# Performance work log

Hardware: AMD Instinct MI355X
Metric: run time of the kernel (lower is better)

## Reference

```python
import jax, jax.numpy as jnp
import numpy as np

B, S, D = 2, 2048, 1024
H = 16
DH = D // H


def setup_inputs() -> dict:
    key = jax.random.key(0)
    ks = jax.random.split(key, 6)
    scale = 1.0 / np.sqrt(D)
    x = jax.random.normal(ks[0], (B, S, D), dtype=jnp.float32)
    Wq = jax.random.normal(ks[1], (D, D), dtype=jnp.float32) * scale
    Wk = jax.random.normal(ks[2], (D, D), dtype=jnp.float32) * scale
    Wv = jax.random.normal(ks[3], (D, D), dtype=jnp.float32) * scale
    Wo = jax.random.normal(ks[4], (D, D), dtype=jnp.float32) * scale
    bo = jax.random.normal(ks[5], (D,), dtype=jnp.float32) * 0.01
    return {"x": x, "Wq": Wq, "Wk": Wk, "Wv": Wv, "Wo": Wo, "bo": bo}


def reference(x, Wq, Wk, Wv, Wo, bo):
    b, t, _ = x.shape
    # project and split heads: [b, h, t, dh]
    q = (x @ Wq).reshape(b, t, H, DH).transpose(0, 2, 1, 3)
    k = (x @ Wk).reshape(b, t, H, DH).transpose(0, 2, 1, 3)
    v = (x @ Wv).reshape(b, t, H, DH).transpose(0, 2, 1, 3)
    scores = jnp.einsum('bhqd,bhkd->bhqk', q, k)
    causal = jnp.triu(jnp.ones((t, t), dtype=bool), k=1)
    scores = jnp.where(causal, -jnp.inf, scores)
    attn = jax.nn.softmax(scores / np.sqrt(DH), axis=-1)
    ctx = jnp.einsum('bhqk,bhkd->bhqd', attn, v)
    ctx = ctx.transpose(0, 2, 1, 3).reshape(b, t, D)
    return ctx @ Wo + bo
```

## Files before the change

kernel.cpp:

```cpp
#include <hip/hip_runtime.h>
#include <hip/hip_bf16.h>

#define B 2
#define S 2048
#define D 1024
#define NH 16
#define DH 64
#define M (B*S)
#define BQ 64
#define BK 64
#define KSCALE 0.18033688011112042f

typedef __hip_bfloat16 bf16;
typedef __attribute__((ext_vector_type(8))) short frag_ab;
typedef __attribute__((ext_vector_type(4))) float frag_cd;
typedef unsigned long long ull;

__device__ __forceinline__ void gload_lds16(const bf16* g, bf16* l) {
    __builtin_amdgcn_global_load_lds((const __attribute__((address_space(1))) unsigned int*)g,
                                     (__attribute__((address_space(3))) unsigned int*)l,
                                     16, 0, 0);
}

__global__ __launch_bounds__(256) void prep(const float* __restrict__ x,  bf16* __restrict__ xb,
                                            const float* __restrict__ W0, const float* __restrict__ W1,
                                            const float* __restrict__ W2, const float* __restrict__ W3,
                                            bf16* __restrict__ T0, bf16* __restrict__ T1,
                                            bf16* __restrict__ T2, bf16* __restrict__ T3) {
    if (blockIdx.z == 4) {
        const int l = blockIdx.y * 32 + blockIdx.x;
        int i = (l * 256 + threadIdx.x) * 4;
#pragma unroll
        for (int rep = 0; rep < 4; rep++, i += 1024 * 256 * 4) {
            const float4 v = *(const float4*)(x + i);
            __align__(8) bf16 t4[4] = {__float2bfloat16(v.x), __float2bfloat16(v.y),
                                       __float2bfloat16(v.z), __float2bfloat16(v.w)};
            *(ull*)(xb + i) = *(const ull*)t4;
        }
        return;
    }
    const float* src; bf16* dst;
    switch (blockIdx.z) {
        case 0: src = W0; dst = T0; break;
        case 1: src = W1; dst = T1; break;
        case 2: src = W2; dst = T2; break;
        default: src = W3; dst = T3; break;
    }
    __shared__ float t[32][33];
    const int tx = threadIdx.x & 31, ty = threadIdx.x >> 5;
    const int c0 = blockIdx.x * 32, r0 = blockIdx.y * 32;
#pragma unroll
    for (int i = 0; i < 4; i++)
        t[ty + 8 * i][tx] = src[(size_t)(r0 + ty + 8 * i) * D + c0 + tx];
    __syncthreads();
#pragma unroll
    for (int i = 0; i < 4; i++)
        dst[(size_t)(c0 + ty + 8 * i) * D + r0 + tx] = __float2bfloat16(t[tx][ty + 8 * i]);
}

__global__ __launch_bounds__(256) void gemm_qkv_all(const bf16* __restrict__ A, const bf16* __restrict__ Bt,
                                                    bf16* __restrict__ Qb, bf16* __restrict__ Kb,
                                                    bf16* __restrict__ Vt_g) {
    __shared__ __align__(16) bf16 As[128 * BK];
    __shared__ __align__(16) bf16 Bs[128 * BK];
    const int tid = threadIdx.x, wave = tid >> 6, lane = tid & 63;
    const int r16 = lane & 15, quad = lane >> 4;
    const int row0 = blockIdx.y * 128;
    const int col0 = blockIdx.x * 128;
    const int wm = (wave & 1) * 64, wn = (wave >> 1) * 64;

    frag_cd acc[4][4];
#pragma unroll
    for (int mt = 0; mt < 4; mt++)
#pragma unroll
        for (int nt = 0; nt < 4; nt++) acc[mt][nt] = frag_cd{0.f, 0.f, 0.f, 0.f};

    for (int k0 = 0; k0 < D; k0 += BK) {
        __syncthreads();
#pragma unroll
        for (int j = 0; j < 4; j++) {
            const int s = wave * 256 + j * 64 + lane;
            const int r = s >> 3;
            const int c = (s ^ r) & 7;
            gload_lds16(A  + (size_t)(row0 + r) * D + k0 + c * 8, &As[(wave * 256 + j * 64) * 8]);
            gload_lds16(Bt + (size_t)(col0 + r) * D + k0 + c * 8, &Bs[(wave * 256 + j * 64) * 8]);
        }
        __syncthreads();

        frag_ab af[4][2], bf[4][2];
#pragma unroll
        for (int mt = 0; mt < 4; mt++) {
            const int row = wm + mt * 16 + r16;
#pragma unroll
            for (int ks = 0; ks < 2; ks++)
                af[mt][ks] = *(const frag_ab*)&As[row * 64 + (((ks * 4 + quad) ^ (row & 7)) * 8)];
        }
#pragma unroll
        for (int nt = 0; nt < 4; nt++) {
            const int row = wn + nt * 16 + r16;
#pragma unroll
            for (int ks = 0; ks < 2; ks++)
                bf[nt][ks] = *(const frag_ab*)&Bs[row * 64 + (((ks * 4 + quad) ^ (row & 7)) * 8)];
        }
#pragma unroll
        for (int mt = 0; mt < 4; mt++)
#pragma unroll
            for (int nt = 0; nt < 4; nt++)
#pragma unroll
                for (int ks = 0; ks < 2; ks++)
                    acc[mt][nt] = __builtin_amdgcn_mfma_f32_16x16x32_bf16(
                        af[mt][ks], bf[nt][ks], acc[mt][nt], 0, 0, 0);
    }

    const int third = col0 >> 10;
    if (third < 2) {
        bf16* Out = (third == 0) ? Qb : Kb;
        const float sc = (third == 0) ? KSCALE : 1.f;
#pragma unroll
        for (int mt = 0; mt < 4; mt++)
#pragma unroll
            for (int nt = 0; nt < 4; nt++) {
                const int cl = (col0 + wn + nt * 16 + r16) & 1023;
#pragma unroll
                for (int rg = 0; rg < 4; rg++) {
                    const int row = row0 + wm + mt * 16 + quad * 4 + rg;
                    Out[(size_t)row * D + cl] = __float2bfloat16(acc[mt][nt][rg] * sc);
                }
            }
    } else {
        const int bb = row0 >> 11;
        const int sb0 = (row0 & 2047) + wm;
#pragma unroll
        for (int mt = 0; mt < 4; mt++)
#pragma unroll
            for (int nt = 0; nt < 4; nt++) {
                const int c  = (col0 + wn + nt * 16 + r16) - 2048;
                const int hh = c >> 6, dl = c & 63;
                const int sb = sb0 + mt * 16 + quad * 4;
                __align__(8) bf16 t4[4];
#pragma unroll
                for (int rg = 0; rg < 4; rg++) t4[rg] = __float2bfloat16(acc[mt][nt][rg]);
                *(ull*)(Vt_g + (((size_t)bb * 16 + hh) * 64 + dl) * S + sb) = *(const ull*)t4;
            }
    }
}

__global__ __launch_bounds__(256) void attn_mfma(const bf16* __restrict__ Q,
                                                 const bf16* __restrict__ K,
                                                 const bf16* __restrict__ Vg,
                                                 bf16* __restrict__ Ctx) {
    __shared__ __align__(16) bf16 Ks[2][BK * DH];
    __shared__ __align__(16) bf16 Vt[2][BK * DH];
    __shared__ __align__(16) bf16 Qs[BQ * DH];
    bf16* Ps = Qs;

    const int tid = threadIdx.x, wave = tid >> 6, lane = tid & 63;
    const int r16 = lane & 15, quad = lane >> 4;
    const int bh = blockIdx.x, jy = blockIdx.y;
    const int qt = (jy < 16) ? jy : 47 - jy;
    const int b = bh >> 4, h = bh & 15;
    const size_t base  = (size_t)b * S * D + (size_t)h * DH;
    const size_t vbase = (size_t)bh * DH * S;
    const int q0 = qt * BQ;
    const int qwave = q0 + wave * 16;
    const int nkt = qt + 1;

#pragma unroll
    for (int j = 0; j < 2; j++) {
        const int s = wave * 128 + j * 64 + lane;
        const int r = s >> 3, c = (s ^ r) & 7;
        gload_lds16(Q + base + (size_t)(q0 + r) * D + c * 8, &Qs[(wave * 128 + j * 64) * 8]);
    }
#pragma unroll
    for (int j = 0; j < 2; j++) {
        const int s = wave * 128 + j * 64 + lane;
        const int r = s >> 3, c = (s ^ r) & 7;
        gload_lds16(K  + base  + (size_t)r * D + c * 8, &Ks[0][(wave * 128 + j * 64) * 8]);
        gload_lds16(Vg + vbase + (size_t)r * S + c * 8, &Vt[0][(wave * 128 + j * 64) * 8]);
    }
    __syncthreads();

    frag_ab qf[2];
    {
        const int row = wave * 16 + r16;
#pragma unroll
        for (int ks = 0; ks < 2; ks++)
            qf[ks] = *(const frag_ab*)&Qs[row * 64 + (((ks * 4 + quad) ^ (row & 7)) * 8)];
    }

    const frag_ab onesf = {(short)0x3F80, (short)0x3F80, (short)0x3F80, (short)0x3F80,
                           (short)0x3F80, (short)0x3F80, (short)0x3F80, (short)0x3F80};

    frag_cd Oacc[4];
#pragma unroll
    for (int nd = 0; nd < 4; nd++) Oacc[nd] = frag_cd{0.f, 0.f, 0.f, 0.f};
    frag_cd Lacc = frag_cd{0.f, 0.f, 0.f, 0.f};

    for (int kt = 0; kt < nkt; kt++) {
        const int k0  = kt * BK;
        const int cur = kt & 1;

        if (kt + 1 < nkt) {
            const int kn = k0 + BK;
#pragma unroll
            for (int j = 0; j < 2; j++) {
                const int s = wave * 128 + j * 64 + lane;
                const int r = s >> 3, c = (s ^ r) & 7;
                gload_lds16(K  + base  + (size_t)(kn + r) * D + c * 8,
                            &Ks[cur ^ 1][(wave * 128 + j * 64) * 8]);
                gload_lds16(Vg + vbase + (size_t)r * S + kn + c * 8,
                            &Vt[cur ^ 1][(wave * 128 + j * 64) * 8]);
            }
        }

        {
            frag_ab ka[4][2];
#pragma unroll
            for (int mk = 0; mk < 4; mk++) {
                const int row = mk * 16 + r16;
#pragma unroll
                for (int ks = 0; ks < 2; ks++)
                    ka[mk][ks] = *(const frag_ab*)&Ks[cur][row * 64 + (((ks * 4 + quad) ^ (row & 7)) * 8)];
            }
            const bool domask = (k0 + BK - 1 > qwave);

            frag_cd Sc[4];
#pragma unroll
            for (int mk = 0; mk < 4; mk++) {
                Sc[mk] = frag_cd{0.f, 0.f, 0.f, 0.f};
#pragma unroll
                for (int ks = 0; ks < 2; ks++)
                    Sc[mk] = __builtin_amdgcn_mfma_f32_16x16x32_bf16(
                        ka[mk][ks], qf[ks], Sc[mk], 0, 0, 0);
            }
            const int qg = qwave + r16;
            const int qrow = wave * 16 + r16;
#pragma unroll
            for (int mk = 0; mk < 4; mk++) {
                __align__(8) bf16 t4[4];
#pragma unroll
                for (int rg = 0; rg < 4; rg++) {
                    float sv = Sc[mk][rg];
                    if (domask) {
                        const int keyg = k0 + mk * 16 + quad * 4 + rg;
                        sv = (keyg <= qg) ? sv : -1e30f;
                    }
                    t4[rg] = __float2bfloat16(__builtin_amdgcn_exp2f(sv));
                }
                const int g2 = (mk * 4 + quad) ^ r16;
                *(ull*)&Ps[qrow * 64 + g2 * 4] = *(const ull*)t4;
            }


            frag_ab pa[2], vb[4][2];
#pragma unroll
            for (int ks = 0; ks < 2; ks++) {
                const int gb = ks * 8 + quad * 2;
                union { ull u[2]; frag_ab f; } t;
                t.u[0] = *(const ull*)&Ps[qrow * 64 + ((gb    ) ^ r16) * 4];
                t.u[1] = *(const ull*)&Ps[qrow * 64 + ((gb + 1) ^ r16) * 4];
                pa[ks] = t.f;
            }
#pragma unroll
            for (int nd = 0; nd < 4; nd++) {
                const int row = nd * 16 + r16;
#pragma unroll
                for (int ks = 0; ks < 2; ks++)
                    vb[nd][ks] = *(const frag_ab*)&Vt[cur][row * 64 + (((ks * 4 + quad) ^ (row & 7)) * 8)];
            }
#pragma unroll
            for (int nd = 0; nd < 4; nd++)
#pragma unroll
                for (int ks = 0; ks < 2; ks++)
                    Oacc[nd] = __builtin_amdgcn_mfma_f32_16x16x32_bf16(
                        vb[nd][ks], pa[ks], Oacc[nd], 0, 0, 0);
#pragma unroll
            for (int ks = 0; ks < 2; ks++)
                Lacc = __builtin_amdgcn_mfma_f32_16x16x32_bf16(
                    onesf, pa[ks], Lacc, 0, 0, 0);
        }

        __syncthreads();
    }

    {
        const float invl = 1.f / Lacc[0];
        const int qg = qwave + r16;
#pragma unroll
        for (int nd = 0; nd < 4; nd++) {
            __align__(8) bf16 t4[4];
#pragma unroll
            for (int rg = 0; rg < 4; rg++)
                t4[rg] = __float2bfloat16(Oacc[nd][rg] * invl);
            *(ull*)(Ctx + base + (size_t)qg * D + nd * 16 + quad * 4) = *(const ull*)t4;
        }
    }
}

__global__ __launch_bounds__(256) void gemm_out64(const bf16* __restrict__ A, const bf16* __restrict__ Bt,
                                                  const float* __restrict__ bias, float* __restrict__ Out) {
    __shared__ __align__(16) bf16 As[2][64 * BK];
    __shared__ __align__(16) bf16 Bs[2][128 * BK];
    const int tid = threadIdx.x, wave = tid >> 6, lane = tid & 63;
    const int r16 = lane & 15, quad = lane >> 4;
    const int row0 = blockIdx.y * 64;
    const int col0 = blockIdx.x * 128;
    const int wm = (wave & 1) * 32, wn = (wave >> 1) * 64;

    frag_cd acc[2][4];
#pragma unroll
    for (int mt = 0; mt < 2; mt++)
#pragma unroll
        for (int nt = 0; nt < 4; nt++) acc[mt][nt] = frag_cd{0.f, 0.f, 0.f, 0.f};

#pragma unroll
    for (int j = 0; j < 2; j++) {
        const int s = wave * 128 + j * 64 + lane;
        const int r = s >> 3, c = (s ^ r) & 7;
        gload_lds16(A + (size_t)(row0 + r) * D + c * 8, &As[0][(wave * 128 + j * 64) * 8]);
    }
#pragma unroll
    for (int j = 0; j < 4; j++) {
        const int s = wave * 256 + j * 64 + lane;
        const int r = s >> 3, c = (s ^ r) & 7;
        gload_lds16(Bt + (size_t)(col0 + r) * D + c * 8, &Bs[0][(wave * 256 + j * 64) * 8]);
    }
    __syncthreads();

    for (int kt = 0; kt < D / BK; kt++) {
        const int cur = kt & 1;
        if (kt + 1 < D / BK) {
            const int kn = (kt + 1) * BK;
#pragma unroll
            for (int j = 0; j < 2; j++) {
                const int s = wave * 128 + j * 64 + lane;
                const int r = s >> 3, c = (s ^ r) & 7;
                gload_lds16(A + (size_t)(row0 + r) * D + kn + c * 8,
                            &As[cur ^ 1][(wave * 128 + j * 64) * 8]);
            }
#pragma unroll
            for (int j = 0; j < 4; j++) {
                const int s = wave * 256 + j * 64 + lane;
                const int r = s >> 3, c = (s ^ r) & 7;
                gload_lds16(Bt + (size_t)(col0 + r) * D + kn + c * 8,
                            &Bs[cur ^ 1][(wave * 256 + j * 64) * 8]);
            }
        }

        frag_ab af[2][2], bf[4][2];
#pragma unroll
        for (int mt = 0; mt < 2; mt++) {
            const int row = wm + mt * 16 + r16;
#pragma unroll
            for (int ks = 0; ks < 2; ks++)
                af[mt][ks] = *(const frag_ab*)&As[cur][row * 64 + (((ks * 4 + quad) ^ (row & 7)) * 8)];
        }
#pragma unroll
        for (int nt = 0; nt < 4; nt++) {
            const int row = wn + nt * 16 + r16;
#pragma unroll
            for (int ks = 0; ks < 2; ks++)
                bf[nt][ks] = *(const frag_ab*)&Bs[cur][row * 64 + (((ks * 4 + quad) ^ (row & 7)) * 8)];
        }
#pragma unroll
        for (int mt = 0; mt < 2; mt++)
#pragma unroll
            for (int nt = 0; nt < 4; nt++)
#pragma unroll
                for (int ks = 0; ks < 2; ks++)
                    acc[mt][nt] = __builtin_amdgcn_mfma_f32_16x16x32_bf16(
                        af[mt][ks], bf[nt][ks], acc[mt][nt], 0, 0, 0);

        __syncthreads();
    }

#pragma unroll
    for (int mt = 0; mt < 2; mt++)
#pragma unroll
        for (int nt = 0; nt < 4; nt++) {
            const int col = col0 + wn + nt * 16 + r16;
            const float bv = bias[col];
#pragma unroll
            for (int rg = 0; rg < 4; rg++) {
                const int row = row0 + wm + mt * 16 + quad * 4 + rg;
                Out[(size_t)row * D + col] = acc[mt][nt][rg] + bv;
            }
        }
}

extern "C" void kernel_launch(void* const* d_in, const int* in_sizes, int n_in,
                              void* d_out, int out_size, void* d_ws, size_t ws_size,
                              hipStream_t stream) {
    const float* x  = (const float*)d_in[0];
    const float* Wq = (const float*)d_in[1];
    const float* Wk = (const float*)d_in[2];
    const float* Wv = (const float*)d_in[3];
    const float* Wo = (const float*)d_in[4];
    const float* bo = (const float*)d_in[5];
    float* out = (float*)d_out;

    bf16* xb    = (bf16*)d_ws;
    bf16* WqkvT = xb    + (size_t)M * D;
    bf16* WoT   = WqkvT + (size_t)3 * D * D;
    bf16* Qb    = WoT   + (size_t)D * D;
    bf16* Kb    = Qb    + (size_t)M * D;
    bf16* Vt_g  = Kb    + (size_t)M * D;
    bf16* Ctxb  = Vt_g  + (size_t)M * D;

    prep<<<dim3(32, 32, 5), 256, 0, stream>>>(x, xb, Wq, Wk, Wv, Wo,
                                              WqkvT, WqkvT + (size_t)D * D,
                                              WqkvT + (size_t)2 * D * D, WoT);
    gemm_qkv_all<<<dim3(24, 32), 256, 0, stream>>>(xb, WqkvT, Qb, Kb, Vt_g);
    attn_mfma<<<dim3(B * NH, S / BQ), 256, 0, stream>>>(Qb, Kb, Vt_g, Ctxb);
    gemm_out64<<<dim3(8, 64), 256, 0, stream>>>(Ctxb, WoT, bo, out);
}
```

Measured before the change: 171.8 us.

## Load K/V fragments directly from global memory instead of LDS double-buffering

The attention kernel drops the shared-memory double-buffered K and V tiles and the Q staging. Each wave now reads its MFMA fragments straight from global memory into registers, and the per-iteration __syncthreads is removed. This cuts LDS traffic, LDS footprint and block-wide barriers, which may allow more blocks per CU. In exchange, the four waves fetch the same K/V tiles redundantly, there is no explicit prefetch, so load latency is hidden only by occupancy, and the global reads are less coalesced.

```diff
diff --git a/kernel.cpp b/kernel.cpp
--- a/kernel.cpp
+++ b/kernel.cpp
@@ -149,10 +149,7 @@
                                                  const bf16* __restrict__ K,
                                                  const bf16* __restrict__ Vg,
                                                  bf16* __restrict__ Ctx) {
-    __shared__ __align__(16) bf16 Ks[2][BK * DH];
-    __shared__ __align__(16) bf16 Vt[2][BK * DH];
-    __shared__ __align__(16) bf16 Qs[BQ * DH];
-    bf16* Ps = Qs;
+    __shared__ __align__(16) bf16 Ps[BQ * DH];
 
     const int tid = threadIdx.x, wave = tid >> 6, lane = tid & 63;
     const int r16 = lane & 15, quad = lane >> 4;
@@ -165,28 +162,16 @@
     const int qwave = q0 + wave * 16;
     const int nkt = qt + 1;
 
-#pragma unroll
-    for (int j = 0; j < 2; j++) {
-        const int s = wave * 128 + j * 64 + lane;
-        const int r = s >> 3, c = (s ^ r) & 7;
-        gload_lds16(Q + base + (size_t)(q0 + r) * D + c * 8, &Qs[(wave * 128 + j * 64) * 8]);
-    }
-#pragma unroll
-    for (int j = 0; j < 2; j++) {
-        const int s = wave * 128 + j * 64 + lane;
-        const int r = s >> 3, c = (s ^ r) & 7;
-        gload_lds16(K  + base  + (size_t)r * D + c * 8, &Ks[0][(wave * 128 + j * 64) * 8]);
-        gload_lds16(Vg + vbase + (size_t)r * S + c * 8, &Vt[0][(wave * 128 + j * 64) * 8]);
-    }
-    __syncthreads();
-
     frag_ab qf[2];
     {
-        const int row = wave * 16 + r16;
+        const bf16* qp = Q + base + (size_t)(qwave + r16) * D + quad * 8;
 #pragma unroll
         for (int ks = 0; ks < 2; ks++)
-            qf[ks] = *(const frag_ab*)&Qs[row * 64 + (((ks * 4 + quad) ^ (row & 7)) * 8)];
-    }
+            qf[ks] = *(const frag_ab*)(qp + ks * 32);
+    }
+
+    const bf16* kp = K  + base  + (size_t)r16 * D + quad * 8;
+    const bf16* vp = Vg + vbase + (size_t)r16 * S + quad * 8;
 
     const frag_ab onesf = {(short)0x3F80, (short)0x3F80, (short)0x3F80, (short)0x3F80,
                            (short)0x3F80, (short)0x3F80, (short)0x3F80, (short)0x3F80};
@@ -197,90 +182,73 @@
     frag_cd Lacc = frag_cd{0.f, 0.f, 0.f, 0.f};
 
     for (int kt = 0; kt < nkt; kt++) {
-        const int k0  = kt * BK;
-        const int cur = kt & 1;
-
-        if (kt + 1 < nkt) {
-            const int kn = k0 + BK;
-#pragma unroll
-            for (int j = 0; j < 2; j++) {
-                const int s = wave * 128 + j * 64 + lane;
-                const int r = s >> 3, c = (s ^ r) & 7;
-                gload_lds16(K  + base  + (size_t)(kn + r) * D + c * 8,
-                            &Ks[cur ^ 1][(wave * 128 + j * 64) * 8]);
-                gload_lds16(Vg + vbase + (size_t)r * S + kn + c * 8,
-                            &Vt[cur ^ 1][(wave * 128 + j * 64) * 8]);
-            }
-        }
-
-        {
-            frag_ab ka[4][2];
-#pragma unroll
-            for (int mk = 0; mk < 4; mk++) {
-                const int row = mk * 16 + r16;
-#pragma unroll
-                for (int ks = 0; ks < 2; ks++)
-                    ka[mk][ks] = *(const frag_ab*)&Ks[cur][row * 64 + (((ks * 4 + quad) ^ (row & 7)) * 8)];
-            }
-            const bool domask = (k0 + BK - 1 > qwave);
-
-            frag_cd Sc[4];
-#pragma unroll
-            for (int mk = 0; mk < 4; mk++) {
-                Sc[mk] = frag_cd{0.f, 0.f, 0.f, 0.f};
-#pragma unroll
-                for (int ks = 0; ks < 2; ks++)
-                    Sc[mk] = __builtin_amdgcn_mfma_f32_16x16x32_bf16(
-                        ka[mk][ks], qf[ks], Sc[mk], 0, 0, 0);
-            }
-            const int qg = qwave + r16;
-            const int qrow = wave * 16 + r16;
-#pragma unroll
-            for (int mk = 0; mk < 4; mk++) {
-                __align__(8) bf16 t4[4];
-#pragma unroll
-                for (int rg = 0; rg < 4; rg++) {
-                    float sv = Sc[mk][rg];
-                    if (domask) {
-                        const int keyg = k0 + mk * 16 + quad * 4 + rg;
-                        sv = (keyg <= qg) ? sv : -1e30f;
-                    }
-                    t4[rg] = __float2bfloat16(__builtin_amdgcn_exp2f(sv));
+        const int k0 = kt * BK;
+
+        frag_ab ka[4][2], vb[4][2];
+#pragma unroll
+        for (int mk = 0; mk < 4; mk++) {
+            const bf16* kr = kp + (size_t)(k0 + mk * 16) * D;
+#pragma unroll
+            for (int ks = 0; ks < 2; ks++)
+                ka[mk][ks] = *(const frag_ab*)(kr + ks * 32);
+        }
+#pragma unroll
+        for (int nd = 0; nd < 4; nd++) {
+            const bf16* vr = vp + (size_t)(nd * 16) * S + k0;
+#pragma unroll
+            for (int ks = 0; ks < 2; ks++)
+                vb[nd][ks] = *(const frag_ab*)(vr + ks * 32);
+        }
+
+        frag_cd Sc[4];
+#pragma unroll
+        for (int mk = 0; mk < 4; mk++) {
+            Sc[mk] = frag_cd{0.f, 0.f, 0.f, 0.f};
+#pragma unroll
+            for (int ks = 0; ks < 2; ks++)
+                Sc[mk] = __builtin_amdgcn_mfma_f32_16x16x32_bf16(
+                    ka[mk][ks], qf[ks], Sc[mk], 0, 0, 0);
+        }
+
+        const bool domask = (k0 + BK - 1 > qwave);
+        const int qg = qwave + r16;
+        const int qrow = wave * 16 + r16;
+#pragma unroll
+        for (int mk = 0; mk < 4; mk++) {
+            __align__(8) bf16 t4[4];
+#pragma unroll
+            for (int rg = 0; rg < 4; rg++) {
+                float sv = Sc[mk][rg];
+                if (domask) {
+                    const int keyg = k0 + mk * 16 + quad * 4 + rg;
+                    sv = (keyg <= qg) ? sv : -1e30f;
                 }
-                const int g2 = (mk * 4 + quad) ^ r16;
-                *(ull*)&Ps[qrow * 64 + g2 * 4] = *(const ull*)t4;
-            }
-
-
-            frag_ab pa[2], vb[4][2];
-#pragma unroll
-            for (int ks = 0; ks < 2; ks++) {
-                const int gb = ks * 8 + quad * 2;
-                union { ull u[2]; frag_ab f; } t;
-                t.u[0] = *(const ull*)&Ps[qrow * 64 + ((gb    ) ^ r16) * 4];
-                t.u[1] = *(const ull*)&Ps[qrow * 64 + ((gb + 1) ^ r16) * 4];
-                pa[ks] = t.f;
-            }
-#pragma unroll
-            for (int nd = 0; nd < 4; nd++) {
-                const int row = nd * 16 + r16;
-#pragma unroll
-                for (int ks = 0; ks < 2; ks++)
-                    vb[nd][ks] = *(const frag_ab*)&Vt[cur][row * 64 + (((ks * 4 + quad) ^ (row & 7)) * 8)];
-            }
-#pragma unroll
-            for (int nd = 0; nd < 4; nd++)
-#pragma unroll
-                for (int ks = 0; ks < 2; ks++)
-                    Oacc[nd] = __builtin_amdgcn_mfma_f32_16x16x32_bf16(
-                        vb[nd][ks], pa[ks], Oacc[nd], 0, 0, 0);
-#pragma unroll
-            for (int ks = 0; ks < 2; ks++)
-                Lacc = __builtin_amdgcn_mfma_f32_16x16x32_bf16(
-                    onesf, pa[ks], Lacc, 0, 0, 0);
-        }
-
-        __syncthreads();
+                t4[rg] = __float2bfloat16(__builtin_amdgcn_exp2f(sv));
+            }
+            const int g2 = (mk * 4 + quad) ^ r16;
+            *(ull*)&Ps[qrow * 64 + g2 * 4] = *(const ull*)t4;
+        }
+
+
+        frag_ab pa[2];
+#pragma unroll
+        for (int ks = 0; ks < 2; ks++) {
+            const int gb = ks * 8 + quad * 2;
+            union { ull u[2]; frag_ab f; } t;
+            t.u[0] = *(const ull*)&Ps[qrow * 64 + ((gb    ) ^ r16) * 4];
+            t.u[1] = *(const ull*)&Ps[qrow * 64 + ((gb + 1) ^ r16) * 4];
+            pa[ks] = t.f;
+        }
+#pragma unroll
+        for (int nd = 0; nd < 4; nd++)
+#pragma unroll
+            for (int ks = 0; ks < 2; ks++)
+                Oacc[nd] = __builtin_amdgcn_mfma_f32_16x16x32_bf16(
+                    vb[nd][ks], pa[ks], Oacc[nd], 0, 0, 0);
+#pragma unroll
+        for (int ks = 0; ks < 2; ks++)
+            Lacc = __builtin_amdgcn_mfma_f32_16x16x32_bf16(
+                onesf, pa[ks], Lacc, 0, 0, 0);
     }
 
     {
```

Result: slower. 251.7 us (+46.5%).

## Split attention work across waves by key slice and reduce outputs in LDS

Applied to the files above, without the earlier changes.

Each wave now owns 16 keys of every K/V tile and computes scores for all 64 queries, instead of owning 16 query rows across all keys. P stays in registers as half-filled MFMA operands, which removes the P store/reload through LDS and the Q staging buffer. Row sums become scalar register accumulation. The four per-wave partial O accumulators are combined through LDS at the end. In exchange, half of each PV MFMA's K dimension is zero padding, the wave uses many more accumulator registers (Oacc grows to 4x4 fragments), and an extra cross-wave reduction with several barriers is added, with a launch-bounds occupancy hint of 3.

```diff
diff --git a/kernel.cpp b/kernel.cpp
--- a/kernel.cpp
+++ b/kernel.cpp
@@ -145,14 +145,13 @@
     }
 }
 
-__global__ __launch_bounds__(256) void attn_mfma(const bf16* __restrict__ Q,
-                                                 const bf16* __restrict__ K,
-                                                 const bf16* __restrict__ Vg,
-                                                 bf16* __restrict__ Ctx) {
+__global__ __launch_bounds__(256, 3) void attn_mfma(const bf16* __restrict__ Q,
+                                                    const bf16* __restrict__ K,
+                                                    const bf16* __restrict__ Vg,
+                                                    bf16* __restrict__ Ctx) {
     __shared__ __align__(16) bf16 Ks[2][BK * DH];
     __shared__ __align__(16) bf16 Vt[2][BK * DH];
-    __shared__ __align__(16) bf16 Qs[BQ * DH];
-    bf16* Ps = Qs;
+    __shared__ float lred[4 * BQ];
 
     const int tid = threadIdx.x, wave = tid >> 6, lane = tid & 63;
     const int r16 = lane & 15, quad = lane >> 4;
@@ -162,15 +161,9 @@
     const size_t base  = (size_t)b * S * D + (size_t)h * DH;
     const size_t vbase = (size_t)bh * DH * S;
     const int q0 = qt * BQ;
-    const int qwave = q0 + wave * 16;
     const int nkt = qt + 1;
-
-#pragma unroll
-    for (int j = 0; j < 2; j++) {
-        const int s = wave * 128 + j * 64 + lane;
-        const int r = s >> 3, c = (s ^ r) & 7;
-        gload_lds16(Q + base + (size_t)(q0 + r) * D + c * 8, &Qs[(wave * 128 + j * 64) * 8]);
-    }
+    const int wkey = wave * 16;
+
 #pragma unroll
     for (int j = 0; j < 2; j++) {
         const int s = wave * 128 + j * 64 + lane;
@@ -178,23 +171,23 @@
         gload_lds16(K  + base  + (size_t)r * D + c * 8, &Ks[0][(wave * 128 + j * 64) * 8]);
         gload_lds16(Vg + vbase + (size_t)r * S + c * 8, &Vt[0][(wave * 128 + j * 64) * 8]);
     }
-    __syncthreads();
-
-    frag_ab qf[2];
-    {
-        const int row = wave * 16 + r16;
+
+    frag_ab qf[4][2];
+#pragma unroll
+    for (int qb = 0; qb < 4; qb++) {
+        const bf16* qp = Q + base + (size_t)(q0 + qb * 16 + r16) * D + quad * 8;
 #pragma unroll
         for (int ks = 0; ks < 2; ks++)
-            qf[ks] = *(const frag_ab*)&Qs[row * 64 + (((ks * 4 + quad) ^ (row & 7)) * 8)];
-    }
-
-    const frag_ab onesf = {(short)0x3F80, (short)0x3F80, (short)0x3F80, (short)0x3F80,
-                           (short)0x3F80, (short)0x3F80, (short)0x3F80, (short)0x3F80};
-
-    frag_cd Oacc[4];
-#pragma unroll
-    for (int nd = 0; nd < 4; nd++) Oacc[nd] = frag_cd{0.f, 0.f, 0.f, 0.f};
-    frag_cd Lacc = frag_cd{0.f, 0.f, 0.f, 0.f};
+            qf[qb][ks] = *(const frag_ab*)(qp + ks * 32);
+    }
+    __syncthreads();
+
+    frag_cd Oacc[4][4];
+#pragma unroll
+    for (int nd = 0; nd < 4; nd++)
+#pragma unroll
+        for (int qb = 0; qb < 4; qb++) Oacc[nd][qb] = frag_cd{0.f, 0.f, 0.f, 0.f};
+    float lsum[4] = {0.f, 0.f, 0.f, 0.f};
 
     for (int kt = 0; kt < nkt; kt++) {
         const int k0  = kt * BK;
@@ -213,87 +206,123 @@
             }
         }
 
-        {
-            frag_ab ka[4][2];
-#pragma unroll
-            for (int mk = 0; mk < 4; mk++) {
-                const int row = mk * 16 + r16;
-#pragma unroll
-                for (int ks = 0; ks < 2; ks++)
-                    ka[mk][ks] = *(const frag_ab*)&Ks[cur][row * 64 + (((ks * 4 + quad) ^ (row & 7)) * 8)];
-            }
-            const bool domask = (k0 + BK - 1 > qwave);
-
-            frag_cd Sc[4];
-#pragma unroll
-            for (int mk = 0; mk < 4; mk++) {
-                Sc[mk] = frag_cd{0.f, 0.f, 0.f, 0.f};
-#pragma unroll
-                for (int ks = 0; ks < 2; ks++)
-                    Sc[mk] = __builtin_amdgcn_mfma_f32_16x16x32_bf16(
-                        ka[mk][ks], qf[ks], Sc[mk], 0, 0, 0);
-            }
-            const int qg = qwave + r16;
-            const int qrow = wave * 16 + r16;
-#pragma unroll
-            for (int mk = 0; mk < 4; mk++) {
+        const int krow = wkey + r16;
+        frag_ab ka[2];
+#pragma unroll
+        for (int ks = 0; ks < 2; ks++)
+            ka[ks] = *(const frag_ab*)&Ks[cur][krow * 64 + (((ks * 4 + quad) ^ (krow & 7)) * 8)];
+
+        frag_ab pbf[4];
+        const int keyg = k0 + wkey + quad * 4;
+#pragma unroll
+        for (int qb = 0; qb < 4; qb++) {
+            frag_cd Sc = frag_cd{0.f, 0.f, 0.f, 0.f};
+#pragma unroll
+            for (int ks = 0; ks < 2; ks++)
+                Sc = __builtin_amdgcn_mfma_f32_16x16x32_bf16(ka[ks], qf[qb][ks], Sc, 0, 0, 0);
+            const bool msk = (k0 + wkey + 15) > (q0 + qb * 16);
+            const int qg = q0 + qb * 16 + r16;
+            float p[4];
+#pragma unroll
+            for (int rg = 0; rg < 4; rg++) {
+                float sv = Sc[rg];
+                if (msk) sv = (keyg + rg <= qg) ? sv : -1e30f;
+                p[rg] = __builtin_amdgcn_exp2f(sv);
+            }
+            lsum[qb] += (p[0] + p[1]) + (p[2] + p[3]);
+            __align__(8) bf16 t4[4] = {__float2bfloat16(p[0]), __float2bfloat16(p[1]),
+                                       __float2bfloat16(p[2]), __float2bfloat16(p[3])};
+            union { ull u[2]; frag_ab f; } tp;
+            tp.u[0] = *(const ull*)t4;
+            tp.u[1] = 0ull;
+            pbf[qb] = tp.f;
+        }
+
+#pragma unroll
+        for (int nd = 0; nd < 4; nd++) {
+            const int vrow = nd * 16 + r16;
+            const int slot = ((wkey + quad * 4) >> 3) ^ (vrow & 7);
+            union { ull u[2]; frag_ab f; } tv;
+            tv.u[0] = *(const ull*)&Vt[cur][vrow * 64 + slot * 8 + (quad & 1) * 4];
+            tv.u[1] = tv.u[0];
+#pragma unroll
+            for (int qb = 0; qb < 4; qb++)
+                Oacc[nd][qb] = __builtin_amdgcn_mfma_f32_16x16x32_bf16(
+                    tv.f, pbf[qb], Oacc[nd][qb], 0, 0, 0);
+        }
+
+        __syncthreads();
+    }
+
+#pragma unroll
+    for (int qb = 0; qb < 4; qb++) {
+        lsum[qb] += __shfl_xor(lsum[qb], 16, 64);
+        lsum[qb] += __shfl_xor(lsum[qb], 32, 64);
+    }
+    if (quad == 0) {
+#pragma unroll
+        for (int qb = 0; qb < 4; qb++)
+            lred[wave * 64 + qb * 16 + r16] = lsum[qb];
+    }
+
+    float* red0 = (float*)&Ks[0][0];
+    float* red1 = (float*)&Vt[0][0];
+    if (wave >= 2) {
+        float* red = (wave == 2) ? red0 : red1;
+#pragma unroll
+        for (int nd = 0; nd < 4; nd++)
+#pragma unroll
+            for (int qb = 0; qb < 4; qb++) {
+                const int idx = (qb * 16 + r16) * 64 + (((nd * 4 + quad) ^ (r16 & 7)) * 4);
+                *(float4*)&red[idx] = float4{Oacc[nd][qb][0], Oacc[nd][qb][1],
+                                             Oacc[nd][qb][2], Oacc[nd][qb][3]};
+            }
+    }
+    __syncthreads();
+    if (wave < 2) {
+        float* red = (wave == 0) ? red0 : red1;
+#pragma unroll
+        for (int nd = 0; nd < 4; nd++)
+#pragma unroll
+            for (int qb = 0; qb < 4; qb++) {
+                const int idx = (qb * 16 + r16) * 64 + (((nd * 4 + quad) ^ (r16 & 7)) * 4);
+                const float4 v = *(const float4*)&red[idx];
+#pragma unroll
+                for (int rg = 0; rg < 4; rg++) Oacc[nd][qb][rg] += ((const float*)&v)[rg];
+            }
+    }
+    __syncthreads();
+    if (wave == 1) {
+#pragma unroll
+        for (int nd = 0; nd < 4; nd++)
+#pragma unroll
+            for (int qb = 0; qb < 4; qb++) {
+                const int idx = (qb * 16 + r16) * 64 + (((nd * 4 + quad) ^ (r16 & 7)) * 4);
+                *(float4*)&red0[idx] = float4{Oacc[nd][qb][0], Oacc[nd][qb][1],
+                                              Oacc[nd][qb][2], Oacc[nd][qb][3]};
+            }
+    }
+    __syncthreads();
+    if (wave == 0) {
+        float lt[4];
+#pragma unroll
+        for (int qb = 0; qb < 4; qb++) {
+            const int qi = qb * 16 + r16;
+            lt[qb] = 1.f / (lred[qi] + lred[64 + qi] + lred[128 + qi] + lred[192 + qi]);
+        }
+#pragma unroll
+        for (int nd = 0; nd < 4; nd++)
+#pragma unroll
+            for (int qb = 0; qb < 4; qb++) {
+                const int idx = (qb * 16 + r16) * 64 + (((nd * 4 + quad) ^ (r16 & 7)) * 4);
+                const float4 v = *(const float4*)&red0[idx];
                 __align__(8) bf16 t4[4];
 #pragma unroll
-                for (int rg = 0; rg < 4; rg++) {
-                    float sv = Sc[mk][rg];
-                    if (domask) {
-                        const int keyg = k0 + mk * 16 + quad * 4 + rg;
-                        sv = (keyg <= qg) ? sv : -1e30f;
-                    }
-                    t4[rg] = __float2bfloat16(__builtin_amdgcn_exp2f(sv));
-                }
-                const int g2 = (mk * 4 + quad) ^ r16;
-                *(ull*)&Ps[qrow * 64 + g2 * 4] = *(const ull*)t4;
-            }
-
-
-            frag_ab pa[2], vb[4][2];
-#pragma unroll
-            for (int ks = 0; ks < 2; ks++) {
-                const int gb = ks * 8 + quad * 2;
-                union { ull u[2]; frag_ab f; } t;
-                t.u[0] = *(const ull*)&Ps[qrow * 64 + ((gb    ) ^ r16) * 4];
-                t.u[1] = *(const ull*)&Ps[qrow * 64 + ((gb + 1) ^ r16) * 4];
-                pa[ks] = t.f;
-            }
-#pragma unroll
-            for (int nd = 0; nd < 4; nd++) {
-                const int row = nd * 16 + r16;
-#pragma unroll
-                for (int ks = 0; ks < 2; ks++)
-                    vb[nd][ks] = *(const frag_ab*)&Vt[cur][row * 64 + (((ks * 4 + quad) ^ (row & 7)) * 8)];
-            }
-#pragma unroll
-            for (int nd = 0; nd < 4; nd++)
-#pragma unroll
-                for (int ks = 0; ks < 2; ks++)
-                    Oacc[nd] = __builtin_amdgcn_mfma_f32_16x16x32_bf16(
-                        vb[nd][ks], pa[ks], Oacc[nd], 0, 0, 0);
-#pragma unroll
-            for (int ks = 0; ks < 2; ks++)
-                Lacc = __builtin_amdgcn_mfma_f32_16x16x32_bf16(
-                    onesf, pa[ks], Lacc, 0, 0, 0);
-        }
-
-        __syncthreads();
-    }
-
-    {
-        const float invl = 1.f / Lacc[0];
-        const int qg = qwave + r16;
-#pragma unroll
-        for (int nd = 0; nd < 4; nd++) {
-            __align__(8) bf16 t4[4];
-#pragma unroll
-            for (int rg = 0; rg < 4; rg++)
-                t4[rg] = __float2bfloat16(Oacc[nd][rg] * invl);
-            *(ull*)(Ctx + base + (size_t)qg * D + nd * 16 + quad * 4) = *(const ull*)t4;
-        }
+                for (int rg = 0; rg < 4; rg++)
+                    t4[rg] = __float2bfloat16((Oacc[nd][qb][rg] + ((const float*)&v)[rg]) * lt[qb]);
+                *(ull*)(Ctx + base + (size_t)(q0 + qb * 16 + r16) * D + nd * 16 + quad * 4) =
+                    *(const ull*)t4;
+            }
     }
 }
 
```

Measured after the change: 179.3 us. 1.04x slower.

## Load V fragments directly from global into registers, bypassing LDS

Applied to the files above, without the earlier changes.

The attention kernel no longer stages the transposed V tile through double-buffered shared memory. Each lane loads its V MFMA operands straight from global memory into registers, and a register double buffer (vbA/vbB, alternated by a two-way unrolled lambda body) prefetches the next tile. This removes the V LDS traffic and halves the LDS footprint, which may raise occupancy. In exchange it adds register pressure and makes the next tile's global loads exposed latency inside the loop.

```diff
diff --git a/kernel.cpp b/kernel.cpp
--- a/kernel.cpp
+++ b/kernel.cpp
@@ -150,7 +150,6 @@
                                                  const bf16* __restrict__ Vg,
                                                  bf16* __restrict__ Ctx) {
     __shared__ __align__(16) bf16 Ks[2][BK * DH];
-    __shared__ __align__(16) bf16 Vt[2][BK * DH];
     __shared__ __align__(16) bf16 Qs[BQ * DH];
     bf16* Ps = Qs;
 
@@ -170,14 +169,15 @@
         const int s = wave * 128 + j * 64 + lane;
         const int r = s >> 3, c = (s ^ r) & 7;
         gload_lds16(Q + base + (size_t)(q0 + r) * D + c * 8, &Qs[(wave * 128 + j * 64) * 8]);
-    }
-#pragma unroll
-    for (int j = 0; j < 2; j++) {
-        const int s = wave * 128 + j * 64 + lane;
-        const int r = s >> 3, c = (s ^ r) & 7;
-        gload_lds16(K  + base  + (size_t)r * D + c * 8, &Ks[0][(wave * 128 + j * 64) * 8]);
-        gload_lds16(Vg + vbase + (size_t)r * S + c * 8, &Vt[0][(wave * 128 + j * 64) * 8]);
-    }
+        gload_lds16(K + base + (size_t)r * D + c * 8, &Ks[0][(wave * 128 + j * 64) * 8]);
+    }
+    const bf16* vp = Vg + vbase + (size_t)r16 * S + quad * 8;
+    frag_ab vbA[4][2], vbB[4][2];
+#pragma unroll
+    for (int nd = 0; nd < 4; nd++)
+#pragma unroll
+        for (int ks = 0; ks < 2; ks++)
+            vbA[nd][ks] = *(const frag_ab*)(vp + (size_t)(nd * 16) * S + ks * 32);
     __syncthreads();
 
     frag_ab qf[2];
@@ -196,7 +196,7 @@
     for (int nd = 0; nd < 4; nd++) Oacc[nd] = frag_cd{0.f, 0.f, 0.f, 0.f};
     frag_cd Lacc = frag_cd{0.f, 0.f, 0.f, 0.f};
 
-    for (int kt = 0; kt < nkt; kt++) {
+    auto BODY = [&](int kt, frag_ab (&vbc)[4][2], frag_ab (&vbn)[4][2]) {
         const int k0  = kt * BK;
         const int cur = kt & 1;
 
@@ -206,81 +206,80 @@
             for (int j = 0; j < 2; j++) {
                 const int s = wave * 128 + j * 64 + lane;
                 const int r = s >> 3, c = (s ^ r) & 7;
-                gload_lds16(K  + base  + (size_t)(kn + r) * D + c * 8,
+                gload_lds16(K + base + (size_t)(kn + r) * D + c * 8,
                             &Ks[cur ^ 1][(wave * 128 + j * 64) * 8]);
-                gload_lds16(Vg + vbase + (size_t)r * S + kn + c * 8,
-                            &Vt[cur ^ 1][(wave * 128 + j * 64) * 8]);
-            }
-        }
-
-        {
-            frag_ab ka[4][2];
-#pragma unroll
-            for (int mk = 0; mk < 4; mk++) {
-                const int row = mk * 16 + r16;
+            }
+#pragma unroll
+            for (int nd = 0; nd < 4; nd++)
 #pragma unroll
                 for (int ks = 0; ks < 2; ks++)
-                    ka[mk][ks] = *(const frag_ab*)&Ks[cur][row * 64 + (((ks * 4 + quad) ^ (row & 7)) * 8)];
-            }
-            const bool domask = (k0 + BK - 1 > qwave);
-
-            frag_cd Sc[4];
-#pragma unroll
-            for (int mk = 0; mk < 4; mk++) {
-                Sc[mk] = frag_cd{0.f, 0.f, 0.f, 0.f};
-#pragma unroll
-                for (int ks = 0; ks < 2; ks++)
-                    Sc[mk] = __builtin_amdgcn_mfma_f32_16x16x32_bf16(
-                        ka[mk][ks], qf[ks], Sc[mk], 0, 0, 0);
-            }
-            const int qg = qwave + r16;
-            const int qrow = wave * 16 + r16;
-#pragma unroll
-            for (int mk = 0; mk < 4; mk++) {
-                __align__(8) bf16 t4[4];
-#pragma unroll
-                for (int rg = 0; rg < 4; rg++) {
-                    float sv = Sc[mk][rg];
-                    if (domask) {
-                        const int keyg = k0 + mk * 16 + quad * 4 + rg;
-                        sv = (keyg <= qg) ? sv : -1e30f;
-                    }
-                    t4[rg] = __float2bfloat16(__builtin_amdgcn_exp2f(sv));
+                    vbn[nd][ks] = *(const frag_ab*)(vp + (size_t)(nd * 16) * S + kn + ks * 32);
+        }
+
+        frag_ab ka[4][2];
+#pragma unroll
+        for (int mk = 0; mk < 4; mk++) {
+            const int row = mk * 16 + r16;
+#pragma unroll
+            for (int ks = 0; ks < 2; ks++)
+                ka[mk][ks] = *(const frag_ab*)&Ks[cur][row * 64 + (((ks * 4 + quad) ^ (row & 7)) * 8)];
+        }
+        const bool domask = (k0 + BK - 1 > qwave);
+
+        frag_cd Sc[4];
+#pragma unroll
+        for (int mk = 0; mk < 4; mk++) {
+            Sc[mk] = frag_cd{0.f, 0.f, 0.f, 0.f};
+#pragma unroll
+            for (int ks = 0; ks < 2; ks++)
+                Sc[mk] = __builtin_amdgcn_mfma_f32_16x16x32_bf16(
+                    ka[mk][ks], qf[ks], Sc[mk], 0, 0, 0);
+        }
+        const int qg = qwave + r16;
+        const int qrow = wave * 16 + r16;
+#pragma unroll
+        for (int mk = 0; mk < 4; mk++) {
+            __align__(8) bf16 t4[4];
+#pragma unroll
+            for (int rg = 0; rg < 4; rg++) {
+                float sv = Sc[mk][rg];
+                if (domask) {
+                    const int keyg = k0 + mk * 16 + quad * 4 + rg;
+                    sv = (keyg <= qg) ? sv : -1e30f;
                 }
-                const int g2 = (mk * 4 + quad) ^ r16;
-                *(ull*)&Ps[qrow * 64 + g2 * 4] = *(const ull*)t4;
-            }
-
-
-            frag_ab pa[2], vb[4][2];
-#pragma unroll
-            for (int ks = 0; ks < 2; ks++) {
-                const int gb = ks * 8 + quad * 2;
-                union { ull u[2]; frag_ab f; } t;
-                t.u[0] = *(const ull*)&Ps[qrow * 64 + ((gb    ) ^ r16) * 4];
-                t.u[1] = *(const ull*)&Ps[qrow * 64 + ((gb + 1) ^ r16) * 4];
-                pa[ks] = t.f;
-            }
-#pragma unroll
-            for (int nd = 0; nd < 4; nd++) {
-                const int row = nd * 16 + r16;
-#pragma unroll
-                for (int ks = 0; ks < 2; ks++)
-                    vb[nd][ks] = *(const frag_ab*)&Vt[cur][row * 64 + (((ks * 4 + quad) ^ (row & 7)) * 8)];
-            }
-#pragma unroll
-            for (int nd = 0; nd < 4; nd++)
-#pragma unroll
-                for (int ks = 0; ks < 2; ks++)
-                    Oacc[nd] = __builtin_amdgcn_mfma_f32_16x16x32_bf16(
-                        vb[nd][ks], pa[ks], Oacc[nd], 0, 0, 0);
-#pragma unroll
-            for (int ks = 0; ks < 2; ks++)
-                Lacc = __builtin_amdgcn_mfma_f32_16x16x32_bf16(
-                    onesf, pa[ks], Lacc, 0, 0, 0);
-        }
+                t4[rg] = __float2bfloat16(__builtin_amdgcn_exp2f(sv));
+            }
+            const int g2 = (mk * 4 + quad) ^ r16;
+            *(ull*)&Ps[qrow * 64 + g2 * 4] = *(const ull*)t4;
+        }
+
+
+        frag_ab pa[2];
+#pragma unroll
+        for (int ks = 0; ks < 2; ks++) {
+            const int gb = ks * 8 + quad * 2;
+            union { ull u[2]; frag_ab f; } t;
+            t.u[0] = *(const ull*)&Ps[qrow * 64 + ((gb    ) ^ r16) * 4];
+            t.u[1] = *(const ull*)&Ps[qrow * 64 + ((gb + 1) ^ r16) * 4];
+            pa[ks] = t.f;
+        }
+#pragma unroll
+        for (int nd = 0; nd < 4; nd++)
+#pragma unroll
+            for (int ks = 0; ks < 2; ks++)
+                Oacc[nd] = __builtin_amdgcn_mfma_f32_16x16x32_bf16(
+                    vbc[nd][ks], pa[ks], Oacc[nd], 0, 0, 0);
+#pragma unroll
+        for (int ks = 0; ks < 2; ks++)
+            Lacc = __builtin_amdgcn_mfma_f32_16x16x32_bf16(
+                onesf, pa[ks], Lacc, 0, 0, 0);
 
         __syncthreads();
+    };
+
+    for (int kt = 0; kt < nkt; ) {
+        BODY(kt, vbA, vbB); kt++;
+        if (kt < nkt) { BODY(kt, vbB, vbA); kt++; }
     }
 
     {
```

New measurement: 208.0 us. +21.1%, slower.
